# Performance work log

Hardware: AMD Instinct MI355X
Metric: run time of the kernel (lower is better)

Reference implementation:

```python
import jax, jax.numpy as jnp
import numpy as np

DIM = 1024
N_HEADS = 16
HEAD_DIM = DIM // N_HEADS
HIDDEN = 4 * DIM
B, T = 4, 2048
EPS = 1e-5


def setup_inputs() -> dict:
    key = jax.random.key(0)
    ks = jax.random.split(key, 12)
    s = lambda fan_in: 1.0 / np.sqrt(fan_in)
    return {
        "x": jax.random.normal(ks[0], (B, T, DIM), jnp.float32),
        "ln1_g": jnp.ones((DIM,), jnp.float32),
        "ln1_b": jnp.zeros((DIM,), jnp.float32),
        "qkv_w": jax.random.normal(ks[1], (DIM, 3 * DIM), jnp.float32) * s(DIM),
        "qkv_b": jnp.zeros((3 * DIM,), jnp.float32),
        "proj_w": jax.random.normal(ks[2], (DIM, DIM), jnp.float32) * s(DIM),
        "proj_b": jnp.zeros((DIM,), jnp.float32),
        "ln2_g": jnp.ones((DIM,), jnp.float32),
        "ln2_b": jnp.zeros((DIM,), jnp.float32),
        "ff1_w": jax.random.normal(ks[3], (DIM, HIDDEN), jnp.float32) * s(DIM),
        "ff1_b": jnp.zeros((HIDDEN,), jnp.float32),
        "ff2_w": jax.random.normal(ks[4], (HIDDEN, DIM), jnp.float32) * s(HIDDEN),
        "ff2_b": jnp.zeros((DIM,), jnp.float32),
    }


def _layernorm(x, g, b):
    mu = jnp.mean(x, axis=-1, keepdims=True)
    var = jnp.mean(jnp.square(x - mu), axis=-1, keepdims=True)
    return (x - mu) * jax.lax.rsqrt(var + EPS) * g + b


def _attn(x, qkv_w, qkv_b, proj_w, proj_b):
    Bx, Tx, C = x.shape
    qkv = (x @ qkv_w + qkv_b).reshape(Bx, Tx, 3, N_HEADS, HEAD_DIM)
    q, k, v = (qkv[:, :, i].transpose(0, 2, 1, 3) for i in range(3))  # [B,H,T,hd]
    att = jnp.einsum('bhqd,bhkd->bhqk', q, k) / np.sqrt(HEAD_DIM)
    causal = jnp.tril(jnp.ones((Tx, Tx), bool))
    att = jnp.where(causal, att, -jnp.inf)
    att = jax.nn.softmax(att, axis=-1)
    out = jnp.einsum('bhqk,bhkd->bhqd', att, v).transpose(0, 2, 1, 3).reshape(Bx, Tx, C)
    return out @ proj_w + proj_b


def reference(x, ln1_g, ln1_b, qkv_w, qkv_b, proj_w, proj_b,
              ln2_g, ln2_b, ff1_w, ff1_b, ff2_w, ff2_b):
    x = x + _attn(_layernorm(x, ln1_g, ln1_b), qkv_w, qkv_b, proj_w, proj_b)
    h = _layernorm(x, ln2_g, ln2_b)
    h = jax.nn.gelu(h @ ff1_w + ff1_b, approximate=False) @ ff2_w + ff2_b
    return x + h
```

## Files before the change

kernel.cpp:

```cpp
#include <hip/hip_runtime.h>
#include <hip/hip_bf16.h>
#include <math.h>

#define DIM 1024
#define NHEADS 16
#define HD 64
#define TT 2048
#define BB 4
#define MTOK (BB*TT)
#define HID 4096

typedef __attribute__((ext_vector_type(8))) short bf16x8;
typedef __attribute__((ext_vector_type(4))) float f32x4;
typedef unsigned short u16;
typedef unsigned int u32;

__device__ inline u16 f2b(float f){
  __hip_bfloat16 h = __float2bfloat16(f);
  return __builtin_bit_cast(u16, h);
}
__device__ inline float b2f(u16 u){
  __hip_bfloat16 h = __builtin_bit_cast(__hip_bfloat16, u);
  return __bfloat162float(h);
}

__device__ inline u32 cvtpk(float lo, float hi_){
  u32 r;
  asm("v_cvt_pk_bf16_f32 %0, %1, %2" : "=v"(r) : "v"(lo), "v"(hi_));
  return r;
}

__device__ inline void load_lds16(const void* g, void* l){
  __builtin_amdgcn_global_load_lds(
      (const __attribute__((address_space(1))) void*)g,
      (__attribute__((address_space(3))) void*)l,
      16, 0, 0);
}

__global__ __launch_bounds__(256) void wconv_t(const float* __restrict__ W,
                                               u16* __restrict__ Wt, int K, int N){
  __shared__ float tl[32][33];
  const int k0 = blockIdx.x*32, n0 = blockIdx.y*32;
  const int tx = threadIdx.x & 31, ty = threadIdx.x >> 5;
  #pragma unroll
  for (int r=0;r<32;r+=8)
    tl[ty+r][tx] = W[(size_t)(k0+ty+r)*N + (n0+tx)];
  __syncthreads();
  #pragma unroll
  for (int r=0;r<32;r+=8)
    Wt[(size_t)(n0+ty+r)*K + (k0+tx)] = f2b(tl[tx][ty+r]);
}

template<bool BF16IN>
__global__ __launch_bounds__(256) void ln_fwd(const float* __restrict__ xf,
                                              const u16* __restrict__ xh,
                                              const float* __restrict__ g,
                                              const float* __restrict__ bta,
                                              u16* __restrict__ out){
  const int row = blockIdx.x, t = threadIdx.x;
  float4 v;
  if constexpr (BF16IN){
    const ushort4 u = ((const ushort4*)(xh + (size_t)row*DIM))[t];
    v.x = b2f(u.x); v.y = b2f(u.y); v.z = b2f(u.z); v.w = b2f(u.w);
  } else {
    v = ((const float4*)(xf + (size_t)row*DIM))[t];
  }
  float s  = v.x+v.y+v.z+v.w;
  float s2 = v.x*v.x+v.y*v.y+v.z*v.z+v.w*v.w;
  #pragma unroll
  for (int m=1;m<64;m<<=1){ s += __shfl_xor(s,m); s2 += __shfl_xor(s2,m); }
  __shared__ float red[8];
  if ((t&63)==0){ red[t>>6]=s; red[4+(t>>6)]=s2; }
  __syncthreads();
  s  = red[0]+red[1]+red[2]+red[3];
  s2 = red[4]+red[5]+red[6]+red[7];
  const float mu = s*(1.0f/DIM);
  const float rstd = rsqrtf(s2*(1.0f/DIM) - mu*mu + 1e-5f);
  const float4 gv = ((const float4*)g)[t];
  const float4 bv = ((const float4*)bta)[t];
  ushort4 ov;
  ov.x = f2b((v.x-mu)*rstd*gv.x + bv.x);
  ov.y = f2b((v.y-mu)*rstd*gv.y + bv.y);
  ov.z = f2b((v.z-mu)*rstd*gv.z + bv.z);
  ov.w = f2b((v.w-mu)*rstd*gv.w + bv.w);
  ((ushort4*)out)[(size_t)row*(DIM/4) + t] = ov;
}

template<int EPI>
__global__ __launch_bounds__(256) void gemm_bt(
    const u16* __restrict__ A, const u16* __restrict__ Bt,
    const float* __restrict__ bias, const float* __restrict__ resid,
    const u16* __restrict__ residh,
    float* __restrict__ outf, u16* __restrict__ outh,
    u16* __restrict__ qo, u16* __restrict__ ko, u16* __restrict__ vo,
    int M, int N, int K)
{
  __shared__ __align__(16) u16 smem[24576];
  u16* Ct = smem;
  const int t = threadIdx.x, wv = t>>6, ln = t&63;
  const int nbx = gridDim.x, nby = gridDim.y;
  const int bid = blockIdx.y*nbx + blockIdx.x;
  const int xcd = bid & 7, lid = bid >> 3;
  const int rpx = nby >> 3;
  const int m0 = (xcd*rpx + (lid % rpx)) * 128;
  const int n0 = (lid / rpx) * 128;
  const int wr = wv>>1, wc = wv&1;
  const int hi = ln>>4, lr = hi*4, lc = ln&15;
  f32x4 acc[4][4] = {};

  auto STAGE32 = [&](int buf, int kt){
    u16* As = smem + buf*8192;
    u16* Bs = smem + buf*8192 + 4096;
    #pragma unroll
    for (int j=0;j<2;j++){
      const int id = j*256 + t;
      const int row = id>>2, c = id&3;
      const int cs = c ^ ((row>>1)&3);
      load_lds16(A  + (size_t)(m0+row)*K + kt + cs*8, (char*)As + id*16);
      load_lds16(Bt + (size_t)(n0+row)*K + kt + cs*8, (char*)Bs + id*16);
    }
  };
  auto RD32 = [&](const u16* base, int r)->bf16x8{
    return *(const bf16x8*)(base + r*32 + ((hi ^ ((r>>1)&3))<<3));
  };
  auto COMPUTE32 = [&](int buf){
    const u16* As = smem + buf*8192;
    const u16* Bs = smem + buf*8192 + 4096;
    bf16x8 af[4], bfr[4];
    #pragma unroll
    for (int mi=0;mi<4;mi++) af[mi] = RD32(As, wr*64 + mi*16 + lc);
    #pragma unroll
    for (int ni=0;ni<4;ni++) bfr[ni] = RD32(Bs, wc*64 + ni*16 + lc);
    __builtin_amdgcn_s_setprio(1);
    #pragma unroll
    for (int mi=0;mi<4;mi++)
      #pragma unroll
      for (int ni=0;ni<4;ni++)
        acc[mi][ni] = __builtin_amdgcn_mfma_f32_16x16x32_bf16(af[mi], bfr[ni], acc[mi][ni], 0,0,0);
    __builtin_amdgcn_s_setprio(0);
  };

  const int nk = K>>5;
  STAGE32(0, 0);
  STAGE32(1, 32);
  asm volatile("s_waitcnt vmcnt(4)" ::: "memory");
  __builtin_amdgcn_s_barrier();
  for (int tt=0; tt<nk; ++tt){
    if (tt+2 < nk) STAGE32((tt+2)%3, (tt+2)<<5);
    COMPUTE32(tt%3);
    if (tt+1 < nk){
      if (tt+2 < nk) asm volatile("s_waitcnt vmcnt(4)" ::: "memory");
      else           asm volatile("s_waitcnt vmcnt(0)" ::: "memory");
      __builtin_amdgcn_s_barrier();
    }
  }

  if constexpr (EPI==3){
    #pragma unroll
    for (int ni=0;ni<4;ni++){
      const int gn = n0 + wc*64 + ni*16 + lc;
      const float bv = bias[gn];
      #pragma unroll
      for (int mi=0;mi<4;mi++){
        const int gmb = m0 + wr*64 + mi*16 + lr;
        f32x4 a = acc[mi][ni];
        #pragma unroll
        for (int i=0;i<4;i++){
          const size_t idx = (size_t)(gmb+i)*DIM + gn;
          outf[idx] = a[i] + bv + b2f(residh[idx]);
        }
      }
    }
  } else {
    const int part = (EPI==0) ? (n0>>10) : 0;
    __syncthreads();
    #pragma unroll
    for (int ni=0;ni<4;ni++){
      const int gn = n0 + wc*64 + ni*16 + lc;
      const float bv = bias[gn];
      const int cl = wc*64 + ni*16 + lc;
      #pragma unroll
      for (int mi=0;mi<4;mi++){
        f32x4 a = acc[mi][ni];
        #pragma unroll
        for (int i=0;i<4;i++){
          const int rl = wr*64 + mi*16 + lr + i;
          float val = a[i] + bv;
          if constexpr (EPI==2){
            const float xx = val*val;
            const float w  = val * fmaf(xx, 0.10294322f, 2.30220781f);
            const float y  = exp2f(w);
            const float r_ = __builtin_amdgcn_rcpf(1.0f + y);
            val = val - val*r_;
          } else if constexpr (EPI==1){
            val += resid[(size_t)(m0+rl)*DIM + gn];
          }
          int r = rl, c = cl;
          if (EPI==0 && part==2){ r = cl; c = rl; }
          const int chunk = c>>3;
          const int csw = (chunk&8) | ((chunk ^ (r&7)) & 7);
          Ct[(r<<7) + (csw<<3) + (c&7)] = f2b(val);
        }
      }
    }
    __syncthreads();
    const int cid = t & 7, rsub = t >> 3;
    const int bb = m0>>11, tok0b = m0&2047;
    const int h0 = (EPI==0) ? ((n0&1023)>>6) : 0;
    #pragma unroll
    for (int pass=0; pass<4; ++pass){
      const int rr = pass*32 + rsub;
      #pragma unroll
      for (int hh=0; hh<2; ++hh){
        const int chunk = hh*8 + cid;
        const int sw = (chunk&8) | ((chunk ^ (rr&7)) & 7);
        const bf16x8 vvv = *(const bf16x8*)&Ct[(rr<<7) + (sw<<3)];
        if constexpr (EPI==2){
          *(bf16x8*)&outh[(size_t)(m0+rr)*HID + n0 + chunk*8] = vvv;
        } else if constexpr (EPI==1){
          *(bf16x8*)&outh[(size_t)(m0+rr)*DIM + n0 + chunk*8] = vvv;
        } else {
          if (part==2){
            const int head = h0 + (rr>>6), d = rr&63;
            *(bf16x8*)&vo[(((size_t)bb*NHEADS + head)*HD + d)*TT + tok0b + chunk*8] = vvv;
          } else {
            u16* dst = part ? ko : qo;
            const int head = h0 + hh;
            *(bf16x8*)&dst[(((size_t)bb*NHEADS + head)*TT + tok0b + rr)*HD + cid*8] = vvv;
          }
        }
      }
    }
  }
}

__global__ __launch_bounds__(512) void attn_fwd(
    const u16* __restrict__ qpt, const u16* __restrict__ kb, const u16* __restrict__ vtb,
    u16* __restrict__ o)
{
  __shared__ __align__(16) u16 Kd[3][64*64];
  __shared__ __align__(16) u16 Vd[3][64*64];
  const int t = threadIdx.x, wv = t>>6, ln = t&63;
  const int bid  = blockIdx.y*gridDim.x + blockIdx.x;
  const int orig = (bid&7)*64 + (bid>>3);
  const int bh   = orig>>3;
  const int qp   = orig&7;
  const int qbA  = qp, qbB = 15-qp;
  const size_t base = (size_t)bh*TT*HD;
  const int hi = ln>>4, lc = ln&15;
  const int ntA = 2*qbA + 2, ntB = 2*qbB + 2;
  const int qbaseA = qbA*128 + wv*16, qrowA = qbaseA + lc;
  const int qbaseB = qbB*128 + wv*16, qrowB = qbaseB + lc;

  const bf16x8 qfA0 = *(const bf16x8*)(qpt + base + (size_t)qrowA*HD + hi*8);
  const bf16x8 qfA1 = *(const bf16x8*)(qpt + base + (size_t)qrowA*HD + 32 + hi*8);
  const bf16x8 qfB0 = *(const bf16x8*)(qpt + base + (size_t)qrowB*HD + hi*8);
  const bf16x8 qfB1 = *(const bf16x8*)(qpt + base + (size_t)qrowB*HD + 32 + hi*8);
  f32x4 oaccA[4] = {}, oaccB[4] = {};
  f32x4 lsumA = {0.f,0.f,0.f,0.f}, lsumB = {0.f,0.f,0.f,0.f};
  float mrunA = -1e30f, mrunB = -1e30f;
  const float SCQ = 0.125f * 1.44269504f;
  bf16x8 ones;
  #pragma unroll
  for (int j=0;j<8;j++) ones[j] = (short)0x3F80;

  const int srow = t>>3;
  const int sch  = t&7;
  const int gch  = (sch ^ (srow&7))<<3;

  auto STAGE = [&](int nb, int kt){
    load_lds16(kb  + base + (size_t)(kt*64+srow)*HD + gch, &Kd[nb][srow*64 + sch*8]);
    load_lds16(vtb + base + (size_t)srow*TT + kt*64 + gch, &Vd[nb][srow*64 + sch*8]);
  };
  auto FRAG = [&](const u16* buf, int r, int ch)->bf16x8{
    return *(const bf16x8*)(buf + r*64 + ((ch ^ (r&7))<<3));
  };
  const int src0 = ((ln&16)<<1) + lc;
  const int src1 = src0 + 16;
  auto pick = [&](u32 w0, u32 w1, int src)->u32{
    const u32 a = (u32)__shfl((int)w0, src);
    const u32 b = (u32)__shfl((int)w1, src);
    return (hi<2) ? a : b;
  };

  auto strip_tile = [&](int kt, const u16* Kb, const u16* Vb,
                        const bf16x8& qf0, const bf16x8& qf1,
                        int qbase, int qrow,
                        f32x4* oacc, f32x4& lsum, float& mrun){
    if (kt*64 > qbase + 15) return;
    float sv[4][4];
    __builtin_amdgcn_s_setprio(1);
    #pragma unroll
    for (int cf=0;cf<4;cf++){
      const int r = cf*16 + lc;
      const bf16x8 kf0 = FRAG(Kb, r, hi);
      const bf16x8 kf1 = FRAG(Kb, r, hi+4);
      f32x4 z = {0.f,0.f,0.f,0.f};
      z = __builtin_amdgcn_mfma_f32_16x16x32_bf16(kf0, qf0, z, 0,0,0);
      z = __builtin_amdgcn_mfma_f32_16x16x32_bf16(kf1, qf1, z, 0,0,0);
      sv[cf][0]=z[0]; sv[cf][1]=z[1]; sv[cf][2]=z[2]; sv[cf][3]=z[3];
    }
    __builtin_amdgcn_s_setprio(0);
    float mx = -1e30f;
    if (kt*64 + 63 > qbase){
      #pragma unroll
      for (int cf=0;cf<4;cf++)
        #pragma unroll
        for (int i=0;i<4;i++){
          const int kvg = kt*64 + cf*16 + 4*hi + i;
          float s_ = sv[cf][i]*SCQ;
          s_ = (kvg > qrow) ? -1e30f : s_;
          sv[cf][i] = s_;
          mx = fmaxf(mx, s_);
        }
    } else {
      #pragma unroll
      for (int cf=0;cf<4;cf++)
        #pragma unroll
        for (int i=0;i<4;i++){
          const float s_ = sv[cf][i]*SCQ;
          sv[cf][i] = s_;
          mx = fmaxf(mx, s_);
        }
    }
    mx = fmaxf(mx, __shfl_xor(mx, 16));
    mx = fmaxf(mx, __shfl_xor(mx, 32));
    if (__any(mx > mrun + 11.0f)){
      const float mnew = fmaxf(mrun, mx);
      const float sc = exp2f(mrun - mnew);
      mrun = mnew;
      const float s0 = __shfl(sc, 4*hi+0);
      const float s1 = __shfl(sc, 4*hi+1);
      const float s2 = __shfl(sc, 4*hi+2);
      const float s3 = __shfl(sc, 4*hi+3);
      #pragma unroll
      for (int df=0;df<4;df++){
        oacc[df][0] *= s0; oacc[df][1] *= s1;
        oacc[df][2] *= s2; oacc[df][3] *= s3;
      }
      lsum[0] *= s0; lsum[1] *= s1; lsum[2] *= s2; lsum[3] *= s3;
    }
    u32 W[4][2];
    #pragma unroll
    for (int cf=0;cf<4;cf++){
      const float e0 = exp2f(sv[cf][0] - mrun);
      const float e1 = exp2f(sv[cf][1] - mrun);
      const float e2 = exp2f(sv[cf][2] - mrun);
      const float e3 = exp2f(sv[cf][3] - mrun);
      W[cf][0] = cvtpk(e0, e1);
      W[cf][1] = cvtpk(e2, e3);
    }
    uint4 uA, uB;
    uA.x = pick(W[0][0], W[1][0], src0);
    uA.y = pick(W[0][1], W[1][1], src0);
    uA.z = pick(W[0][0], W[1][0], src1);
    uA.w = pick(W[0][1], W[1][1], src1);
    uB.x = pick(W[2][0], W[3][0], src0);
    uB.y = pick(W[2][1], W[3][1], src0);
    uB.z = pick(W[2][0], W[3][0], src1);
    uB.w = pick(W[2][1], W[3][1], src1);
    const bf16x8 paA = __builtin_bit_cast(bf16x8, uA);
    const bf16x8 paB = __builtin_bit_cast(bf16x8, uB);
    __builtin_amdgcn_s_setprio(1);
    #pragma unroll
    for (int df=0;df<4;df++){
      const bf16x8 v0 = FRAG(Vb, df*16+lc, hi);
      const bf16x8 v1 = FRAG(Vb, df*16+lc, hi+4);
      oacc[df] = __builtin_amdgcn_mfma_f32_16x16x32_bf16(paA, v0, oacc[df], 0,0,0);
      oacc[df] = __builtin_amdgcn_mfma_f32_16x16x32_bf16(paB, v1, oacc[df], 0,0,0);
    }
    lsum = __builtin_amdgcn_mfma_f32_16x16x32_bf16(paA, ones, lsum, 0,0,0);
    lsum = __builtin_amdgcn_mfma_f32_16x16x32_bf16(paB, ones, lsum, 0,0,0);
    __builtin_amdgcn_s_setprio(0);
  };

  STAGE(0, 0);
  STAGE(1, 1);
  asm volatile("s_waitcnt vmcnt(2)" ::: "memory");
  __syncthreads();

  for (int kt=0; kt<ntB; kt++){
    if (kt+2 < ntB) STAGE((kt+2)%3, kt+2);
    const u16* Kb = Kd[kt%3];
    const u16* Vb = Vd[kt%3];
    strip_tile(kt, Kb, Vb, qfB0, qfB1, qbaseB, qrowB, oaccB, lsumB, mrunB);
    if (kt < ntA)
      strip_tile(kt, Kb, Vb, qfA0, qfA1, qbaseA, qrowA, oaccA, lsumA, mrunA);
    if (kt+1 < ntB){
      if (kt+2 < ntB) asm volatile("s_waitcnt vmcnt(2)" ::: "memory");
      else            asm volatile("s_waitcnt vmcnt(0)" ::: "memory");
      __syncthreads();
    }
  }

  const int b = bh>>4, h = bh&15;
  {
    const float inv[4] = {1.0f/lsumA[0], 1.0f/lsumA[1], 1.0f/lsumA[2], 1.0f/lsumA[3]};
    const int qg0 = qbaseA + 4*hi;
    #pragma unroll
    for (int i=0;i<4;i++){
      const size_t rowb = ((size_t)b*TT + (size_t)(qg0 + i))*DIM + h*HD;
      #pragma unroll
      for (int df=0;df<4;df++)
        o[rowb + df*16 + lc] = f2b(oaccA[df][i]*inv[i]);
    }
  }
  {
    const float inv[4] = {1.0f/lsumB[0], 1.0f/lsumB[1], 1.0f/lsumB[2], 1.0f/lsumB[3]};
    const int qg0 = qbaseB + 4*hi;
    #pragma unroll
    for (int i=0;i<4;i++){
      const size_t rowb = ((size_t)b*TT + (size_t)(qg0 + i))*DIM + h*HD;
      #pragma unroll
      for (int df=0;df<4;df++)
        o[rowb + df*16 + lc] = f2b(oaccB[df][i]*inv[i]);
    }
  }
}

extern "C" void kernel_launch(void* const* d_in, const int* in_sizes, int n_in,
                              void* d_out, int out_size, void* d_ws, size_t ws_size,
                              hipStream_t stream){
  (void)in_sizes; (void)n_in; (void)out_size; (void)ws_size;
  const float* x     = (const float*)d_in[0];
  const float* ln1g  = (const float*)d_in[1];
  const float* ln1b  = (const float*)d_in[2];
  const float* qkvw  = (const float*)d_in[3];
  const float* qkvb  = (const float*)d_in[4];
  const float* projw = (const float*)d_in[5];
  const float* projb = (const float*)d_in[6];
  const float* ln2g  = (const float*)d_in[7];
  const float* ln2b  = (const float*)d_in[8];
  const float* ff1w  = (const float*)d_in[9];
  const float* ff1b  = (const float*)d_in[10];
  const float* ff2w  = (const float*)d_in[11];
  const float* ff2b  = (const float*)d_in[12];
  float* out = (float*)d_out;

  char* ws = (char*)d_ws;
  size_t off = 0;
  auto alloc = [&](size_t n){ char* p = ws + off; off += (n + 255) & ~(size_t)255; return p; };
  u16* wqkvt  = (u16*)alloc((size_t)3072*1024*2);
  u16* wprojt = (u16*)alloc((size_t)1024*1024*2);
  u16* wff1t  = (u16*)alloc((size_t)4096*1024*2);
  u16* wff2t  = (u16*)alloc((size_t)1024*4096*2);
  u16* h1     = (u16*)alloc((size_t)MTOK*DIM*2);
  u16* qbuf   = (u16*)alloc((size_t)MTOK*DIM*2);
  u16* kbuf   = (u16*)alloc((size_t)MTOK*DIM*2);
  u16* vbuf   = (u16*)alloc((size_t)MTOK*DIM*2);
  u16* aout   = (u16*)alloc((size_t)MTOK*DIM*2);
  u16* x2h    = (u16*)alloc((size_t)MTOK*DIM*2);
  u16* h2     = (u16*)alloc((size_t)MTOK*DIM*2);
  u16* act    = (u16*)alloc((size_t)MTOK*HID*2);

  wconv_t<<<dim3(1024/32, 3072/32), 256, 0, stream>>>(qkvw, wqkvt, 1024, 3072);
  wconv_t<<<dim3(1024/32, 1024/32), 256, 0, stream>>>(projw, wprojt, 1024, 1024);
  wconv_t<<<dim3(1024/32, 4096/32), 256, 0, stream>>>(ff1w, wff1t, 1024, 4096);
  wconv_t<<<dim3(4096/32, 1024/32), 256, 0, stream>>>(ff2w, wff2t, 4096, 1024);

  ln_fwd<false><<<MTOK, 256, 0, stream>>>(x, nullptr, ln1g, ln1b, h1);

  gemm_bt<0><<<dim3(3072/128, MTOK/128), 256, 0, stream>>>(
      h1, wqkvt, qkvb, nullptr, nullptr, nullptr, nullptr, qbuf, kbuf, vbuf, MTOK, 3072, 1024);

  attn_fwd<<<dim3(8, BB*NHEADS), 512, 0, stream>>>(qbuf, kbuf, vbuf, aout);

  gemm_bt<1><<<dim3(1024/128, MTOK/128), 256, 0, stream>>>(
      aout, wprojt, projb, x, nullptr, nullptr, x2h, nullptr, nullptr, nullptr, MTOK, 1024, 1024);

  ln_fwd<true><<<MTOK, 256, 0, stream>>>(nullptr, x2h, ln2g, ln2b, h2);

  gemm_bt<2><<<dim3(4096/128, MTOK/128), 256, 0, stream>>>(
      h2, wff1t, ff1b, nullptr, nullptr, nullptr, act, nullptr, nullptr, nullptr, MTOK, HID, 1024);

  gemm_bt<3><<<dim3(1024/128, MTOK/128), 256, 0, stream>>>(
      act, wff2t, ff2b, nullptr, x2h, out, nullptr, nullptr, nullptr, nullptr, MTOK, DIM, HID);
}
```

Baseline: 396.8 us.

## Use wider 128x256 GEMM tile with triple buffering for QKV and FF1

Adds a gemm_w kernel with a 128x256 output tile (each wave computes 64x128), a three-stage LDS pipeline with K-step 32, and s_setprio around the MFMA block. The QKV and FF1 projections use it, which raises operand reuse per loaded byte and cuts the number of blocks. The epilogue writes out the two 128-column halves in sequence through shared memory. In exchange it uses more registers and LDS (occupancy hint of 2 blocks per CU), and the grid is half as large.

Measured after the change: 418.9 us. 5.6% more time.

```diff
diff --git a/kernel.cpp b/kernel.cpp
--- a/kernel.cpp
+++ b/kernel.cpp
@@ -87,12 +87,146 @@
 }
 
 template<int EPI>
+__global__ __launch_bounds__(256, 2) void gemm_w(
+    const u16* __restrict__ A, const u16* __restrict__ Bt,
+    const float* __restrict__ bias, u16* __restrict__ outh,
+    u16* __restrict__ qo, u16* __restrict__ ko, u16* __restrict__ vo,
+    int K)
+{
+  __shared__ __align__(16) u16 smem[36864];
+  u16* Ct = smem;
+  const int t = threadIdx.x, wv = t>>6, ln = t&63;
+  const int nbx = gridDim.x, nby = gridDim.y;
+  const int bid = blockIdx.y*nbx + blockIdx.x;
+  const int xcd = bid & 7, lid = bid >> 3;
+  const int rpx = nby >> 3;
+  const int m0 = (xcd*rpx + (lid % rpx)) * 128;
+  const int n0 = (lid / rpx) * 256;
+  const int wr = wv>>1, wc = wv&1;
+  const int hi = ln>>4, lr = hi*4, lc = ln&15;
+  f32x4 acc[4][8] = {};
+
+  auto STAGE = [&](int buf, int kt){
+    u16* As = smem + buf*12288;
+    u16* Bs = smem + buf*12288 + 4096;
+    #pragma unroll
+    for (int j=0;j<2;j++){
+      const int id = j*256 + t;
+      const int row = id>>2, c = id&3;
+      const int cs = c ^ ((row>>1)&3);
+      load_lds16(A + (size_t)(m0+row)*K + kt + cs*8, (char*)As + id*16);
+    }
+    #pragma unroll
+    for (int j=0;j<4;j++){
+      const int id = j*256 + t;
+      const int row = id>>2, c = id&3;
+      const int cs = c ^ ((row>>1)&3);
+      load_lds16(Bt + (size_t)(n0+row)*K + kt + cs*8, (char*)Bs + id*16);
+    }
+  };
+  auto RD32 = [&](const u16* base, int r)->bf16x8{
+    return *(const bf16x8*)(base + r*32 + ((hi ^ ((r>>1)&3))<<3));
+  };
+  auto COMPUTE = [&](int buf){
+    const u16* As = smem + buf*12288;
+    const u16* Bs = smem + buf*12288 + 4096;
+    bf16x8 af[4], bfr[8];
+    #pragma unroll
+    for (int mi=0;mi<4;mi++) af[mi] = RD32(As, wr*64 + mi*16 + lc);
+    #pragma unroll
+    for (int ni=0;ni<8;ni++) bfr[ni] = RD32(Bs, wc*128 + ni*16 + lc);
+    __builtin_amdgcn_s_setprio(1);
+    #pragma unroll
+    for (int mi=0;mi<4;mi++)
+      #pragma unroll
+      for (int ni=0;ni<8;ni++)
+        acc[mi][ni] = __builtin_amdgcn_mfma_f32_16x16x32_bf16(af[mi], bfr[ni], acc[mi][ni], 0,0,0);
+    __builtin_amdgcn_s_setprio(0);
+  };
+
+  const int nk = K>>5;
+  STAGE(0, 0);
+  STAGE(1, 32);
+  asm volatile("s_waitcnt vmcnt(6)" ::: "memory");
+  __builtin_amdgcn_s_barrier();
+  for (int tt=0; tt<nk; ++tt){
+    if (tt+2 < nk) STAGE((tt+2)%3, (tt+2)<<5);
+    COMPUTE(tt%3);
+    if (tt+1 < nk){
+      if (tt+2 < nk) asm volatile("s_waitcnt vmcnt(6)" ::: "memory");
+      else           asm volatile("s_waitcnt vmcnt(0)" ::: "memory");
+      __builtin_amdgcn_s_barrier();
+    }
+  }
+
+  const int bb = m0>>11, tok0b = m0&2047;
+  #pragma unroll
+  for (int ch=0; ch<2; ++ch){
+    const int part = (EPI==0) ? ((n0 + ch*128)>>10) : 0;
+    const int h0 = ((n0 + ch*128)&1023)>>6;
+    __syncthreads();
+    if (wc == ch){
+      #pragma unroll
+      for (int ni=0;ni<8;ni++){
+        const int gn = n0 + wc*128 + ni*16 + lc;
+        const float bv = bias[gn];
+        const int cl = ni*16 + lc;
+        #pragma unroll
+        for (int mi=0;mi<4;mi++){
+          f32x4 a = acc[mi][ni];
+          #pragma unroll
+          for (int i=0;i<4;i++){
+            const int rl = wr*64 + mi*16 + lr + i;
+            float val = a[i] + bv;
+            if constexpr (EPI==2){
+              const float xx = val*val;
+              const float w  = val * fmaf(xx, 0.10294322f, 2.30220781f);
+              const float y  = exp2f(w);
+              const float r_ = __builtin_amdgcn_rcpf(1.0f + y);
+              val = val - val*r_;
+            }
+            int r = rl, c = cl;
+            if (EPI==0 && part==2){ r = cl; c = rl; }
+            const int chunk = c>>3;
+            const int csw = (chunk&8) | ((chunk ^ (r&7)) & 7);
+            Ct[(r<<7) + (csw<<3) + (c&7)] = f2b(val);
+          }
+        }
+      }
+    }
+    __syncthreads();
+    const int cid = t & 7, rsub = t >> 3;
+    #pragma unroll
+    for (int pass=0; pass<4; ++pass){
+      const int rr = pass*32 + rsub;
+      #pragma unroll
+      for (int hh=0; hh<2; ++hh){
+        const int chunk = hh*8 + cid;
+        const int sw = (chunk&8) | ((chunk ^ (rr&7)) & 7);
+        const bf16x8 vvv = *(const bf16x8*)&Ct[(rr<<7) + (sw<<3)];
+        if constexpr (EPI==2){
+          *(bf16x8*)&outh[(size_t)(m0+rr)*HID + n0 + ch*128 + chunk*8] = vvv;
+        } else {
+          if (part==2){
+            const int head = h0 + (rr>>6), d = rr&63;
+            *(bf16x8*)&vo[(((size_t)bb*NHEADS + head)*HD + d)*TT + tok0b + chunk*8] = vvv;
+          } else {
+            u16* dst = part ? ko : qo;
+            const int head = h0 + hh;
+            *(bf16x8*)&dst[(((size_t)bb*NHEADS + head)*TT + tok0b + rr)*HD + cid*8] = vvv;
+          }
+        }
+      }
+    }
+  }
+}
+
+template<int EPI>
 __global__ __launch_bounds__(256) void gemm_bt(
     const u16* __restrict__ A, const u16* __restrict__ Bt,
     const float* __restrict__ bias, const float* __restrict__ resid,
     const u16* __restrict__ residh,
     float* __restrict__ outf, u16* __restrict__ outh,
-    u16* __restrict__ qo, u16* __restrict__ ko, u16* __restrict__ vo,
     int M, int N, int K)
 {
   __shared__ __align__(16) u16 smem[24576];
@@ -172,7 +306,6 @@
       }
     }
   } else {
-    const int part = (EPI==0) ? (n0>>10) : 0;
     __syncthreads();
     #pragma unroll
     for (int ni=0;ni<4;ni++){
@@ -185,28 +318,15 @@
         #pragma unroll
         for (int i=0;i<4;i++){
           const int rl = wr*64 + mi*16 + lr + i;
-          float val = a[i] + bv;
-          if constexpr (EPI==2){
-            const float xx = val*val;
-            const float w  = val * fmaf(xx, 0.10294322f, 2.30220781f);
-            const float y  = exp2f(w);
-            const float r_ = __builtin_amdgcn_rcpf(1.0f + y);
-            val = val - val*r_;
-          } else if constexpr (EPI==1){
-            val += resid[(size_t)(m0+rl)*DIM + gn];
-          }
-          int r = rl, c = cl;
-          if (EPI==0 && part==2){ r = cl; c = rl; }
-          const int chunk = c>>3;
-          const int csw = (chunk&8) | ((chunk ^ (r&7)) & 7);
-          Ct[(r<<7) + (csw<<3) + (c&7)] = f2b(val);
+          float val = a[i] + bv + resid[(size_t)(m0+rl)*DIM + gn];
+          const int chunk = cl>>3;
+          const int csw = (chunk&8) | ((chunk ^ (rl&7)) & 7);
+          Ct[(rl<<7) + (csw<<3) + (cl&7)] = f2b(val);
         }
       }
     }
     __syncthreads();
     const int cid = t & 7, rsub = t >> 3;
-    const int bb = m0>>11, tok0b = m0&2047;
-    const int h0 = (EPI==0) ? ((n0&1023)>>6) : 0;
     #pragma unroll
     for (int pass=0; pass<4; ++pass){
       const int rr = pass*32 + rsub;
@@ -215,20 +335,7 @@
         const int chunk = hh*8 + cid;
         const int sw = (chunk&8) | ((chunk ^ (rr&7)) & 7);
         const bf16x8 vvv = *(const bf16x8*)&Ct[(rr<<7) + (sw<<3)];
-        if constexpr (EPI==2){
-          *(bf16x8*)&outh[(size_t)(m0+rr)*HID + n0 + chunk*8] = vvv;
-        } else if constexpr (EPI==1){
-          *(bf16x8*)&outh[(size_t)(m0+rr)*DIM + n0 + chunk*8] = vvv;
-        } else {
-          if (part==2){
-            const int head = h0 + (rr>>6), d = rr&63;
-            *(bf16x8*)&vo[(((size_t)bb*NHEADS + head)*HD + d)*TT + tok0b + chunk*8] = vvv;
-          } else {
-            u16* dst = part ? ko : qo;
-            const int head = h0 + hh;
-            *(bf16x8*)&dst[(((size_t)bb*NHEADS + head)*TT + tok0b + rr)*HD + cid*8] = vvv;
-          }
-        }
+        *(bf16x8*)&outh[(size_t)(m0+rr)*DIM + n0 + chunk*8] = vvv;
       }
     }
   }
@@ -460,19 +567,19 @@
 
   ln_fwd<false><<<MTOK, 256, 0, stream>>>(x, nullptr, ln1g, ln1b, h1);
 
-  gemm_bt<0><<<dim3(3072/128, MTOK/128), 256, 0, stream>>>(
-      h1, wqkvt, qkvb, nullptr, nullptr, nullptr, nullptr, qbuf, kbuf, vbuf, MTOK, 3072, 1024);
+  gemm_w<0><<<dim3(3072/256, MTOK/128), 256, 0, stream>>>(
+      h1, wqkvt, qkvb, nullptr, qbuf, kbuf, vbuf, 1024);
 
   attn_fwd<<<dim3(8, BB*NHEADS), 512, 0, stream>>>(qbuf, kbuf, vbuf, aout);
 
   gemm_bt<1><<<dim3(1024/128, MTOK/128), 256, 0, stream>>>(
-      aout, wprojt, projb, x, nullptr, nullptr, x2h, nullptr, nullptr, nullptr, MTOK, 1024, 1024);
+      aout, wprojt, projb, x, nullptr, nullptr, x2h, MTOK, 1024, 1024);
 
   ln_fwd<true><<<MTOK, 256, 0, stream>>>(nullptr, x2h, ln2g, ln2b, h2);
 
-  gemm_bt<2><<<dim3(4096/128, MTOK/128), 256, 0, stream>>>(
-      h2, wff1t, ff1b, nullptr, nullptr, nullptr, act, nullptr, nullptr, nullptr, MTOK, HID, 1024);
+  gemm_w<2><<<dim3(4096/256, MTOK/128), 256, 0, stream>>>(
+      h2, wff1t, ff1b, act, nullptr, nullptr, nullptr, 1024);
 
   gemm_bt<3><<<dim3(1024/128, MTOK/128), 256, 0, stream>>>(
-      act, wff2t, ff2b, nullptr, x2h, out, nullptr, nullptr, nullptr, nullptr, MTOK, DIM, HID);
-}
+      act, wff2t, ff2b, nullptr, x2h, out, nullptr, MTOK, DIM, HID);
+}
```
